# Performance work log

Hardware: AMD Instinct MI355X
Metric: run time of the kernel (lower is better)

## Reference

```python
import jax, jax.numpy as jnp
import numpy as np

B, S, D, H = 2, 4096, 768, 12
HD = D // H  # head_dim = 64


def setup_inputs() -> dict:
    key = jax.random.key(0)
    ks = jax.random.split(key, 12)
    s = 0.02
    inp = {
        'q': jax.random.normal(ks[0], (B, S, D), jnp.float32),
        'k': jax.random.normal(ks[1], (B, S, D), jnp.float32),
        'v': jax.random.normal(ks[2], (B, S, D), jnp.float32),
        # True = masked position (filled with -inf); causal mask, broadcastable
        'mask': jnp.triu(jnp.ones((S, S), jnp.bool_), k=1)[None, None],
        'Wq': jax.random.normal(ks[3], (D, D), jnp.float32) * s,
        'bq': jnp.zeros((D,), jnp.float32),
        'Wk': jax.random.normal(ks[4], (D, D), jnp.float32) * s,
        'bk': jnp.zeros((D,), jnp.float32),
        'Wv': jax.random.normal(ks[5], (D, D), jnp.float32) * s,
        'bv': jnp.zeros((D,), jnp.float32),
        'Wo': jax.random.normal(ks[6], (D, D), jnp.float32) * s,
        'bo': jnp.zeros((D,), jnp.float32),
    }
    return inp


def _split_heads(x):
    # [B, S, D] -> [B, H, S, HD]
    return x.reshape(B, S, H, HD).transpose(0, 2, 1, 3)


def reference(q, k, v, mask, Wq, bq, Wk, bk, Wv, bv, Wo, bo):
    # per-head linear projections (torch Linear: x @ W.T + b)
    qh = _split_heads(q @ Wq.T + bq)
    kh = _split_heads(k @ Wk.T + bk)
    vh = _split_heads(v @ Wv.T + bv)
    scale = 1.0 / np.sqrt(HD).astype(np.float32)
    # naive full [B, H, S, S] attention scores (module materializes these)
    wei = jnp.einsum('bhqd,bhkd->bhqk', qh, kh) * scale
    wei = jnp.where(mask, -jnp.inf, wei)
    attn = jax.nn.softmax(wei, axis=-1)
    feats = jnp.einsum('bhqk,bhkd->bhqd', attn, vh)
    # concat heads: [B, H, S, HD] -> [B, S, D]
    out = feats.transpose(0, 2, 1, 3).reshape(B, S, D)
    return out @ Wo.T + bo
```

## Files before the change

kernel.cpp:

```cpp
#include <hip/hip_runtime.h>
#include <math.h>

#define B_  2
#define S_  4096
#define D_  768
#define H_  12
#define HD_ 64

using bf16x8  = __attribute__((ext_vector_type(8))) __bf16;
using f32x4   = __attribute__((ext_vector_type(4))) float;
using ushort8 = __attribute__((ext_vector_type(8))) unsigned short;

__device__ __forceinline__ unsigned short f2b(float f) {
    union { float f; unsigned u; } x; x.f = f;
    unsigned r = x.u + 0x7fffu + ((x.u >> 16) & 1u);
    return (unsigned short)(r >> 16);
}
__device__ __forceinline__ unsigned pk2(float x, float y) {
    unsigned ux = __builtin_bit_cast(unsigned, x) + 0x8000u;
    unsigned uy = __builtin_bit_cast(unsigned, y) + 0x8000u;
    return (uy & 0xFFFF0000u) | (ux >> 16);
}

__global__ __launch_bounds__(256)
void w_convert(const float* __restrict__ Wq, const float* __restrict__ Wk,
               const float* __restrict__ Wv, const float* __restrict__ Wo,
               unsigned short* __restrict__ Wb)
{
    const int z = blockIdx.y;
    const float* src = (z == 0) ? Wq : (z == 1) ? Wk : (z == 2) ? Wv : Wo;
    unsigned short* dst = Wb + (size_t)z * (D_ * D_);
    int idx = blockIdx.x * 256 + threadIdx.x;
    const float4 a = *(const float4*)(src + (size_t)idx * 8);
    const float4 b = *(const float4*)(src + (size_t)idx * 8 + 4);
    uint4 o;
    o.x = pk2(a.x, a.y); o.y = pk2(a.z, a.w);
    o.z = pk2(b.x, b.y); o.w = pk2(b.z, b.w);
    *(uint4*)(dst + (size_t)idx * 8) = o;
}

__global__ __launch_bounds__(256)
void qkv_gemm(const float* __restrict__ q, const float* __restrict__ k,
              const float* __restrict__ v,
              const unsigned short* __restrict__ Wb,
              const float* __restrict__ bq, const float* __restrict__ bk,
              const float* __restrict__ bv,
              unsigned short* __restrict__ Qp, unsigned short* __restrict__ Kp,
              unsigned short* __restrict__ Vrm)
{
    constexpr int BM = 128, BN = 128, BK = 32, LDP = 40;
    const int z = blockIdx.z;
    const float* A    = (z == 0) ? q  : (z == 1) ? k  : v;
    const unsigned short* W = Wb + (size_t)z * (D_ * D_);
    const float* bias = (z == 0) ? bq : (z == 1) ? bk : bv;
    unsigned short* C = (z == 0) ? Qp : (z == 1) ? Kp : Vrm;

    __shared__ __align__(16) unsigned short As[BM * LDP];
    __shared__ __align__(16) unsigned short Bs[BN * LDP];

    const int tid = threadIdx.x, bm = blockIdx.x, bn = blockIdx.y;
    const int w = tid >> 6, lane = tid & 63, lr = lane & 15, lg = lane >> 4;
    const int wm = (w >> 1) * 64, wn = (w & 1) * 64;

    f32x4 acc[4][4] = {};

    for (int k0 = 0; k0 < D_; k0 += BK) {
        __syncthreads();
        for (int t = 0; t < 4; ++t) {
            int idx = tid + t * 256, row = idx >> 3, c4 = (idx & 7) * 4;
            float4 va = *(const float4*)(A + (size_t)(bm * BM + row) * D_ + k0 + c4);
            *(uint2*)&As[row * LDP + c4] = make_uint2(pk2(va.x, va.y), pk2(va.z, va.w));
        }
        for (int t = 0; t < 2; ++t) {
            int idx = tid + t * 256, row = idx >> 2, c8 = (idx & 3) * 8;
            *(ushort8*)&Bs[row * LDP + c8] =
                *(const ushort8*)(W + (size_t)(bn * BN + row) * D_ + k0 + c8);
        }
        __syncthreads();
        bf16x8 af[4], bfr[4];
        for (int i = 0; i < 4; ++i) af[i]  = *(const bf16x8*)&As[(wm + i * 16 + lr) * LDP + lg * 8];
        for (int j = 0; j < 4; ++j) bfr[j] = *(const bf16x8*)&Bs[(wn + j * 16 + lr) * LDP + lg * 8];
        for (int i = 0; i < 4; ++i)
            for (int j = 0; j < 4; ++j)
                acc[i][j] = __builtin_amdgcn_mfma_f32_16x16x32_bf16(af[i], bfr[j], acc[i][j], 0, 0, 0);
    }

    const float qscale = 0.18033688011112042f;
    for (int i = 0; i < 4; ++i) {
        int row0 = bm * BM + wm + i * 16 + lg * 4;
        for (int j = 0; j < 4; ++j) {
            int col = bn * BN + wn + j * 16 + lr;
            float bv_ = bias[col];
            for (int r = 0; r < 4; ++r) {
                float val = acc[i][j][r] + bv_;
                if (z == 0) val *= qscale;
                C[(size_t)(row0 + r) * D_ + col] = f2b(val);
            }
        }
    }
}

__global__ __launch_bounds__(256)
void v_transpose(const unsigned short* __restrict__ Vrm,
                 unsigned short* __restrict__ Vt)
{
    __shared__ __align__(16) unsigned short T[64][72];
    const int st = blockIdx.x, bh = blockIdx.y;
    const int b = bh / H_, h = bh % H_;
    const int tid = threadIdx.x;

    for (int t = 0; t < 2; ++t) {
        int idx = tid + t * 256, s = idx >> 3, c8 = (idx & 7) * 8;
        *(ushort8*)&T[s][c8] =
            *(const ushort8*)(Vrm + ((size_t)(b * S_ + st * 64 + s)) * D_ + h * HD_ + c8);
    }
    __syncthreads();
    const int d = tid >> 2;
    for (int it = 0; it < 2; ++it) {
        int s8 = (tid & 3) + it * 4;
        ushort8 val;
        for (int j = 0; j < 8; ++j) val[j] = T[s8 * 8 + j][d];
        *(ushort8*)(Vt + ((size_t)bh * HD_ + d) * S_ + st * 64 + s8 * 8) = val;
    }
}

__global__ __launch_bounds__(256)
void o_gemm(const unsigned short* __restrict__ Ai, const unsigned short* __restrict__ W,
            const float* __restrict__ bias, float* __restrict__ C)
{
    constexpr int BM = 128, BN = 64, BK = 32, LDP = 40;
    __shared__ __align__(16) unsigned short As[BM * LDP];
    __shared__ __align__(16) unsigned short Bs[BN * LDP];

    const int tid = threadIdx.x, bm = blockIdx.x, bn = blockIdx.y;
    const int w = tid >> 6, lane = tid & 63, lr = lane & 15, lg = lane >> 4;
    const int wm = (w >> 1) * 64, wn = (w & 1) * 32;

    f32x4 acc[4][2] = {};

    for (int k0 = 0; k0 < D_; k0 += BK) {
        __syncthreads();
        for (int t = 0; t < 2; ++t) {
            int idx = tid + t * 256, row = idx >> 2, c8 = (idx & 3) * 8;
            *(ushort8*)&As[row * LDP + c8] =
                *(const ushort8*)(Ai + (size_t)(bm * BM + row) * D_ + k0 + c8);
        }
        {
            int row = tid >> 2, c8 = (tid & 3) * 8;
            *(ushort8*)&Bs[row * LDP + c8] =
                *(const ushort8*)(W + (size_t)(bn * BN + row) * D_ + k0 + c8);
        }
        __syncthreads();
        bf16x8 af[4], bfr[2];
        for (int i = 0; i < 4; ++i) af[i]  = *(const bf16x8*)&As[(wm + i * 16 + lr) * LDP + lg * 8];
        for (int j = 0; j < 2; ++j) bfr[j] = *(const bf16x8*)&Bs[(wn + j * 16 + lr) * LDP + lg * 8];
        for (int i = 0; i < 4; ++i)
            for (int j = 0; j < 2; ++j)
                acc[i][j] = __builtin_amdgcn_mfma_f32_16x16x32_bf16(af[i], bfr[j], acc[i][j], 0, 0, 0);
    }

    for (int i = 0; i < 4; ++i) {
        int row0 = bm * BM + wm + i * 16 + lg * 4;
        for (int j = 0; j < 2; ++j) {
            int col = bn * BN + wn + j * 16 + lr;
            float bv_ = bias[col];
            for (int r = 0; r < 4; ++r)
                C[(size_t)(row0 + r) * D_ + col] = acc[i][j][r] + bv_;
        }
    }
}

__global__ __launch_bounds__(256)
void attn_kernel(const unsigned short* __restrict__ Qp,
                 const unsigned short* __restrict__ Kp,
                 const unsigned short* __restrict__ Vt,
                 unsigned short* __restrict__ feats)
{
    __shared__ __align__(16) unsigned short Ks[64 * 72];
    __shared__ __align__(16) unsigned short Vs[64 * 72];
    __shared__ __align__(16) unsigned short Ps[4][2][16 * 72];

    const int tid = threadIdx.x;
    const int lin = blockIdx.x + gridDim.x * blockIdx.y;
    const int xcd = lin & 7, idx = lin >> 3;
    const int bh  = xcd * 3 + (idx >> 5);
    const int p   = idx & 31;
    const int b = bh / H_, h = bh % H_;
    const int w = tid >> 6, lane = tid & 63, lr = lane & 15, lg = lane >> 4;

    const int qtA = 63 - p, qtB = p;

    bf16x8 ones;
    for (int j = 0; j < 8; ++j) ones[j] = (__bf16)1.0f;

    const size_t kbase = ((size_t)b * S_) * D_ + h * HD_;
    const size_t vbase = ((size_t)bh * HD_) * S_;

    const size_t qbA = ((size_t)(b * S_ + qtA * 64 + w * 16 + lr)) * D_ + h * HD_;
    const size_t qbB = ((size_t)(b * S_ + qtB * 64 + w * 16 + lr)) * D_ + h * HD_;
    bf16x8 qfA0 = *(const bf16x8*)(Qp + qbA + lg * 8);
    bf16x8 qfA1 = *(const bf16x8*)(Qp + qbA + 32 + lg * 8);
    bf16x8 qfB0 = *(const bf16x8*)(Qp + qbB + lg * 8);
    bf16x8 qfB1 = *(const bf16x8*)(Qp + qbB + 32 + lg * 8);

    f32x4 oA[4] = {}, oB[4] = {};
    f32x4 lA = {0.f, 0.f, 0.f, 0.f}, lB = {0.f, 0.f, 0.f, 0.f};

    const int nst = qtA + 1;

    for (int kb = 0; kb < nst; ++kb) {
        const bool bAct = (kb <= qtB);
        __syncthreads();
        for (int t = 0; t < 2; ++t) {
            int id2 = tid + t * 256, row = id2 >> 3, c8 = (id2 & 7) * 8;
            *(ushort8*)&Ks[row * 72 + c8] =
                *(const ushort8*)(Kp + kbase + (size_t)(kb * 64 + row) * D_ + c8);
            *(ushort8*)&Vs[row * 72 + c8] =
                *(const ushort8*)(Vt + vbase + (size_t)row * S_ + kb * 64 + c8);
        }
        __syncthreads();

        bf16x8 kf[4][2];
        for (int n = 0; n < 4; ++n) {
            kf[n][0] = *(const bf16x8*)&Ks[(n * 16 + lr) * 72 + lg * 8];
            kf[n][1] = *(const bf16x8*)&Ks[(n * 16 + lr) * 72 + 32 + lg * 8];
        }

        {
            f32x4 st[4];
            for (int n = 0; n < 4; ++n) {
                f32x4 s = {0.f, 0.f, 0.f, 0.f};
                s = __builtin_amdgcn_mfma_f32_16x16x32_bf16(kf[n][0], qfA0, s, 0, 0, 0);
                s = __builtin_amdgcn_mfma_f32_16x16x32_bf16(kf[n][1], qfA1, s, 0, 0, 0);
                st[n] = s;
            }
            if (kb == qtA) {
                for (int n = 0; n < 4; ++n)
                    for (int r = 0; r < 4; ++r)
                        if (n * 16 + lg * 4 + r > w * 16 + lr) st[n][r] = -INFINITY;
            }
            for (int n = 0; n < 4; ++n) {
                float e0 = __builtin_amdgcn_exp2f(st[n][0]);
                float e1 = __builtin_amdgcn_exp2f(st[n][1]);
                float e2 = __builtin_amdgcn_exp2f(st[n][2]);
                float e3 = __builtin_amdgcn_exp2f(st[n][3]);
                *(uint2*)&Ps[w][0][lr * 72 + n * 16 + lg * 4] =
                    make_uint2(pk2(e0, e1), pk2(e2, e3));
            }
        }
        if (bAct) {
            f32x4 st[4];
            for (int n = 0; n < 4; ++n) {
                f32x4 s = {0.f, 0.f, 0.f, 0.f};
                s = __builtin_amdgcn_mfma_f32_16x16x32_bf16(kf[n][0], qfB0, s, 0, 0, 0);
                s = __builtin_amdgcn_mfma_f32_16x16x32_bf16(kf[n][1], qfB1, s, 0, 0, 0);
                st[n] = s;
            }
            if (kb == qtB) {
                for (int n = 0; n < 4; ++n)
                    for (int r = 0; r < 4; ++r)
                        if (n * 16 + lg * 4 + r > w * 16 + lr) st[n][r] = -INFINITY;
            }
            for (int n = 0; n < 4; ++n) {
                float e0 = __builtin_amdgcn_exp2f(st[n][0]);
                float e1 = __builtin_amdgcn_exp2f(st[n][1]);
                float e2 = __builtin_amdgcn_exp2f(st[n][2]);
                float e3 = __builtin_amdgcn_exp2f(st[n][3]);
                *(uint2*)&Ps[w][1][lr * 72 + n * 16 + lg * 4] =
                    make_uint2(pk2(e0, e1), pk2(e2, e3));
            }
        }
        __asm__ volatile("" ::: "memory");

        bf16x8 vf[4][2];
        for (int n = 0; n < 4; ++n) {
            vf[n][0] = *(const bf16x8*)&Vs[(n * 16 + lr) * 72 + lg * 8];
            vf[n][1] = *(const bf16x8*)&Vs[(n * 16 + lr) * 72 + 32 + lg * 8];
        }
        {
            bf16x8 pf0 = *(const bf16x8*)&Ps[w][0][lr * 72 + lg * 8];
            bf16x8 pf1 = *(const bf16x8*)&Ps[w][0][lr * 72 + 32 + lg * 8];
            for (int n = 0; n < 4; ++n) {
                oA[n] = __builtin_amdgcn_mfma_f32_16x16x32_bf16(vf[n][0], pf0, oA[n], 0, 0, 0);
                oA[n] = __builtin_amdgcn_mfma_f32_16x16x32_bf16(vf[n][1], pf1, oA[n], 0, 0, 0);
            }
            lA = __builtin_amdgcn_mfma_f32_16x16x32_bf16(ones, pf0, lA, 0, 0, 0);
            lA = __builtin_amdgcn_mfma_f32_16x16x32_bf16(ones, pf1, lA, 0, 0, 0);
        }
        if (bAct) {
            bf16x8 pf0 = *(const bf16x8*)&Ps[w][1][lr * 72 + lg * 8];
            bf16x8 pf1 = *(const bf16x8*)&Ps[w][1][lr * 72 + 32 + lg * 8];
            for (int n = 0; n < 4; ++n) {
                oB[n] = __builtin_amdgcn_mfma_f32_16x16x32_bf16(vf[n][0], pf0, oB[n], 0, 0, 0);
                oB[n] = __builtin_amdgcn_mfma_f32_16x16x32_bf16(vf[n][1], pf1, oB[n], 0, 0, 0);
            }
            lB = __builtin_amdgcn_mfma_f32_16x16x32_bf16(ones, pf0, lB, 0, 0, 0);
            lB = __builtin_amdgcn_mfma_f32_16x16x32_bf16(ones, pf1, lB, 0, 0, 0);
        }
    }

    {
        const float inv = 1.0f / lA[0];
        const size_t obase = ((size_t)(b * S_ + qtA * 64 + w * 16 + lr)) * D_ + h * HD_;
        for (int n = 0; n < 4; ++n) {
            unsigned short e0 = f2b(oA[n][0] * inv), e1 = f2b(oA[n][1] * inv);
            unsigned short e2 = f2b(oA[n][2] * inv), e3 = f2b(oA[n][3] * inv);
            *(uint2*)(feats + obase + n * 16 + lg * 4) =
                make_uint2((unsigned)e0 | ((unsigned)e1 << 16),
                           (unsigned)e2 | ((unsigned)e3 << 16));
        }
    }
    {
        const float inv = 1.0f / lB[0];
        const size_t obase = ((size_t)(b * S_ + qtB * 64 + w * 16 + lr)) * D_ + h * HD_;
        for (int n = 0; n < 4; ++n) {
            unsigned short e0 = f2b(oB[n][0] * inv), e1 = f2b(oB[n][1] * inv);
            unsigned short e2 = f2b(oB[n][2] * inv), e3 = f2b(oB[n][3] * inv);
            *(uint2*)(feats + obase + n * 16 + lg * 4) =
                make_uint2((unsigned)e0 | ((unsigned)e1 << 16),
                           (unsigned)e2 | ((unsigned)e3 << 16));
        }
    }
}

extern "C" void kernel_launch(void* const* d_in, const int* in_sizes, int n_in,
                              void* d_out, int out_size, void* d_ws, size_t ws_size,
                              hipStream_t stream) {
    const float* q  = (const float*)d_in[0];
    const float* k  = (const float*)d_in[1];
    const float* v  = (const float*)d_in[2];
    const float* Wq = (const float*)d_in[4];
    const float* bq = (const float*)d_in[5];
    const float* Wk = (const float*)d_in[6];
    const float* bk = (const float*)d_in[7];
    const float* Wv = (const float*)d_in[8];
    const float* bv = (const float*)d_in[9];
    const float* Wo = (const float*)d_in[10];
    const float* bo = (const float*)d_in[11];
    float* out = (float*)d_out;

    const size_t npro = (size_t)B_ * S_ * D_;
    const size_t nw   = (size_t)D_ * D_;
    unsigned short* Qp    = (unsigned short*)d_ws;
    unsigned short* Kp    = Qp + npro;
    unsigned short* Vrm   = Kp + npro;
    unsigned short* Vt    = Vrm + npro;
    unsigned short* Wb    = Vt + npro;
    unsigned short* feats = Vrm;

    dim3 blk(256);
    w_convert<<<dim3(288, 4), blk, 0, stream>>>(Wq, Wk, Wv, Wo, Wb);
    qkv_gemm<<<dim3(64, 6, 3), blk, 0, stream>>>(q, k, v, Wb, bq, bk, bv,
                                                 Qp, Kp, Vrm);
    v_transpose<<<dim3(S_ / 64, B_ * H_), blk, 0, stream>>>(Vrm, Vt);
    attn_kernel<<<dim3(32, B_ * H_), blk, 0, stream>>>(Qp, Kp, Vt, feats);
    o_gemm<<<dim3(64, 12), blk, 0, stream>>>(feats, Wb + 3 * nw, bo, out);
}
```

Measured before the change: 368.8 us.

## Prefetch next K/V tile into registers and raise wave priority around MFMAs

The K/V tile for the next iteration is now loaded from global memory into registers right after the shared-memory barrier, so the global loads overlap with this iteration's MFMA and exp work instead of stalling at the top of each loop. V fragments are read from LDS early, alongside the K fragments. s_setprio is raised around the MFMA blocks so waves issuing matrix work get scheduling priority. This costs extra registers for the prefetch buffers and the early V fragments, which may reduce occupancy.

```diff
diff --git a/kernel.cpp b/kernel.cpp
--- a/kernel.cpp
+++ b/kernel.cpp
@@ -208,32 +208,55 @@
 
     const int nst = qtA + 1;
 
+    const int srow = tid >> 3, sc8 = (tid & 7) * 8;
+    const unsigned short* kptr = Kp + kbase + (size_t)srow * D_ + sc8;
+    const unsigned short* vptr = Vt + vbase + (size_t)srow * S_ + sc8;
+    unsigned short* KsW = &Ks[srow * 72 + sc8];
+    unsigned short* VsW = &Vs[srow * 72 + sc8];
+
+    ushort8 kr0 = *(const ushort8*)(kptr);
+    ushort8 kr1 = *(const ushort8*)(kptr + (size_t)32 * D_);
+    ushort8 vr0 = *(const ushort8*)(vptr);
+    ushort8 vr1 = *(const ushort8*)(vptr + (size_t)32 * S_);
+
     for (int kb = 0; kb < nst; ++kb) {
         const bool bAct = (kb <= qtB);
         __syncthreads();
-        for (int t = 0; t < 2; ++t) {
-            int id2 = tid + t * 256, row = id2 >> 3, c8 = (id2 & 7) * 8;
-            *(ushort8*)&Ks[row * 72 + c8] =
-                *(const ushort8*)(Kp + kbase + (size_t)(kb * 64 + row) * D_ + c8);
-            *(ushort8*)&Vs[row * 72 + c8] =
-                *(const ushort8*)(Vt + vbase + (size_t)row * S_ + kb * 64 + c8);
-        }
-        __syncthreads();
-
-        bf16x8 kf[4][2];
+        *(ushort8*)KsW            = kr0;
+        *(ushort8*)(KsW + 32*72)  = kr1;
+        *(ushort8*)VsW            = vr0;
+        *(ushort8*)(VsW + 32*72)  = vr1;
+        __syncthreads();
+
+        if (kb + 1 < nst) {
+            kptr += (size_t)64 * D_;
+            vptr += 64;
+            kr0 = *(const ushort8*)(kptr);
+            kr1 = *(const ushort8*)(kptr + (size_t)32 * D_);
+            vr0 = *(const ushort8*)(vptr);
+            vr1 = *(const ushort8*)(vptr + (size_t)32 * S_);
+        }
+
+        bf16x8 kf[4][2], vf[4][2];
         for (int n = 0; n < 4; ++n) {
             kf[n][0] = *(const bf16x8*)&Ks[(n * 16 + lr) * 72 + lg * 8];
             kf[n][1] = *(const bf16x8*)&Ks[(n * 16 + lr) * 72 + 32 + lg * 8];
         }
+        for (int n = 0; n < 4; ++n) {
+            vf[n][0] = *(const bf16x8*)&Vs[(n * 16 + lr) * 72 + lg * 8];
+            vf[n][1] = *(const bf16x8*)&Vs[(n * 16 + lr) * 72 + 32 + lg * 8];
+        }
 
         {
             f32x4 st[4];
+            __builtin_amdgcn_s_setprio(1);
             for (int n = 0; n < 4; ++n) {
                 f32x4 s = {0.f, 0.f, 0.f, 0.f};
                 s = __builtin_amdgcn_mfma_f32_16x16x32_bf16(kf[n][0], qfA0, s, 0, 0, 0);
                 s = __builtin_amdgcn_mfma_f32_16x16x32_bf16(kf[n][1], qfA1, s, 0, 0, 0);
                 st[n] = s;
             }
+            __builtin_amdgcn_s_setprio(0);
             if (kb == qtA) {
                 for (int n = 0; n < 4; ++n)
                     for (int r = 0; r < 4; ++r)
@@ -250,12 +273,14 @@
         }
         if (bAct) {
             f32x4 st[4];
+            __builtin_amdgcn_s_setprio(1);
             for (int n = 0; n < 4; ++n) {
                 f32x4 s = {0.f, 0.f, 0.f, 0.f};
                 s = __builtin_amdgcn_mfma_f32_16x16x32_bf16(kf[n][0], qfB0, s, 0, 0, 0);
                 s = __builtin_amdgcn_mfma_f32_16x16x32_bf16(kf[n][1], qfB1, s, 0, 0, 0);
                 st[n] = s;
             }
+            __builtin_amdgcn_s_setprio(0);
             if (kb == qtB) {
                 for (int n = 0; n < 4; ++n)
                     for (int r = 0; r < 4; ++r)
@@ -272,30 +297,29 @@
         }
         __asm__ volatile("" ::: "memory");
 
-        bf16x8 vf[4][2];
-        for (int n = 0; n < 4; ++n) {
-            vf[n][0] = *(const bf16x8*)&Vs[(n * 16 + lr) * 72 + lg * 8];
-            vf[n][1] = *(const bf16x8*)&Vs[(n * 16 + lr) * 72 + 32 + lg * 8];
-        }
         {
             bf16x8 pf0 = *(const bf16x8*)&Ps[w][0][lr * 72 + lg * 8];
             bf16x8 pf1 = *(const bf16x8*)&Ps[w][0][lr * 72 + 32 + lg * 8];
+            __builtin_amdgcn_s_setprio(1);
             for (int n = 0; n < 4; ++n) {
                 oA[n] = __builtin_amdgcn_mfma_f32_16x16x32_bf16(vf[n][0], pf0, oA[n], 0, 0, 0);
                 oA[n] = __builtin_amdgcn_mfma_f32_16x16x32_bf16(vf[n][1], pf1, oA[n], 0, 0, 0);
             }
             lA = __builtin_amdgcn_mfma_f32_16x16x32_bf16(ones, pf0, lA, 0, 0, 0);
             lA = __builtin_amdgcn_mfma_f32_16x16x32_bf16(ones, pf1, lA, 0, 0, 0);
+            __builtin_amdgcn_s_setprio(0);
         }
         if (bAct) {
             bf16x8 pf0 = *(const bf16x8*)&Ps[w][1][lr * 72 + lg * 8];
             bf16x8 pf1 = *(const bf16x8*)&Ps[w][1][lr * 72 + 32 + lg * 8];
+            __builtin_amdgcn_s_setprio(1);
             for (int n = 0; n < 4; ++n) {
                 oB[n] = __builtin_amdgcn_mfma_f32_16x16x32_bf16(vf[n][0], pf0, oB[n], 0, 0, 0);
                 oB[n] = __builtin_amdgcn_mfma_f32_16x16x32_bf16(vf[n][1], pf1, oB[n], 0, 0, 0);
             }
             lB = __builtin_amdgcn_mfma_f32_16x16x32_bf16(ones, pf0, lB, 0, 0, 0);
             lB = __builtin_amdgcn_mfma_f32_16x16x32_bf16(ones, pf1, lB, 0, 0, 0);
+            __builtin_amdgcn_s_setprio(0);
         }
     }
 
```

Result: slower. 376.3 us (+2.0%).
